# Kernel tuning notes

Hardware: AMD Instinct MI355X
Metric: run time of the kernel (lower is better)

## Reference

```python
import jax, jax.numpy as jnp
import numpy as np

# Mamba3/SSD selective state-space mixer (scalar-A-per-head SSD recurrence,
# causal depthwise conv on x/B/C, gated RMSNorm, in/out projections).
D_MODEL = 1024
EXPAND = 2
D_INNER = EXPAND * D_MODEL            # 2048
HEADDIM = D_MODEL // 16               # 64  (head_count=16 -> headdim 64)
NHEADS = D_INNER // HEADDIM           # 32
D_STATE = 128
CONV_W = 4
CONV_DIM = D_INNER + 2 * D_STATE      # x, B, C share the conv
D_IN_PROJ = 2 * D_INNER + 2 * D_STATE + NHEADS  # z, x, B, C, dt
EPS = 1e-5


def setup_inputs() -> dict:
    key = jax.random.key(0)
    ks = jax.random.split(key, 8)
    B, L = 4, 2048
    hidden = jax.random.normal(ks[0], (B, L, D_MODEL), dtype=jnp.float32)
    W_in = jax.random.normal(ks[1], (D_MODEL, D_IN_PROJ), dtype=jnp.float32) * 0.02
    conv_w = jax.random.normal(ks[2], (CONV_DIM, CONV_W), dtype=jnp.float32) * 0.2
    conv_b = jnp.zeros((CONV_DIM,), dtype=jnp.float32)
    # dt_bias: inverse-softplus of dt ~ U[1e-3, 0.1]
    dt = jnp.exp(jax.random.uniform(ks[3], (NHEADS,)) * (np.log(0.1) - np.log(1e-3)) + np.log(1e-3))
    dt_bias = dt + jnp.log(-jnp.expm1(-dt))
    A_log = jnp.log(jax.random.uniform(ks[4], (NHEADS,), minval=1.0, maxval=16.0))
    D = jnp.ones((NHEADS,), dtype=jnp.float32)
    norm_w = jnp.ones((D_INNER,), dtype=jnp.float32)
    W_out = jax.random.normal(ks[5], (D_INNER, D_MODEL), dtype=jnp.float32) * 0.02
    return {"hidden": hidden, "W_in": W_in, "conv_w": conv_w, "conv_b": conv_b,
            "dt_bias": dt_bias, "A_log": A_log, "D": D, "norm_w": norm_w, "W_out": W_out}


def _silu(x):
    return x * jax.nn.sigmoid(x)


def _mixer(hidden, W_in, conv_w, conv_b, dt_bias, A_log, D, norm_w, W_out):
    Bsz, L, _ = hidden.shape
    zxbcdt = hidden @ W_in                                    # [B,L,D_IN_PROJ]
    z = zxbcdt[..., :D_INNER]
    xBC = zxbcdt[..., D_INNER:D_INNER + CONV_DIM]
    dt = zxbcdt[..., -NHEADS:]                                # [B,L,H]
    # causal depthwise conv, width 4 (small fixed loop over taps)
    xp = jnp.pad(xBC, ((0, 0), (CONV_W - 1, 0), (0, 0)))
    conv = sum(xp[:, k:k + L, :] * conv_w[:, k] for k in range(CONV_W))
    xBC = _silu(conv + conv_b)
    x = xBC[..., :D_INNER].reshape(Bsz, L, NHEADS, HEADDIM)   # [B,L,H,P]
    Bm = xBC[..., D_INNER:D_INNER + D_STATE]                  # [B,L,N]
    Cm = xBC[..., D_INNER + D_STATE:]                         # [B,L,N]
    dt = jax.nn.softplus(dt + dt_bias)                        # [B,L,H]
    dA = jnp.exp(dt * (-jnp.exp(A_log)))                      # [B,L,H] decay in (0,1)
    dBx = jnp.einsum('blh,bln,blhp->blhpn', dt, Bm, x)        # [B,L,H,P,N]

    def step(h, inp):
        dA_t, dBx_t, C_t = inp                                # [B,H],[B,H,P,N],[B,N]
        h = dA_t[:, :, None, None] * h + dBx_t
        y = jnp.einsum('bhpn,bn->bhp', h, C_t)
        return h, y

    h0 = jnp.zeros((Bsz, NHEADS, HEADDIM, D_STATE), dtype=hidden.dtype)
    xs = (jnp.moveaxis(dA, 1, 0), jnp.moveaxis(dBx, 1, 0), jnp.moveaxis(Cm, 1, 0))
    _, ys = jax.lax.scan(step, h0, xs)                        # [L,B,H,P]
    y = jnp.moveaxis(ys, 0, 1) + D[None, None, :, None] * x   # skip term
    y = y.reshape(Bsz, L, D_INNER)
    # gated RMSNorm: norm(y * silu(z))
    y = y * _silu(z)
    y = y * jax.lax.rsqrt(jnp.mean(y * y, axis=-1, keepdims=True) + EPS) * norm_w
    return y @ W_out


def reference(hidden, W_in, conv_w, conv_b, dt_bias, A_log, D, norm_w, W_out):
    return _mixer(hidden, W_in, conv_w, conv_b, dt_bias, A_log, D, norm_w, W_out)
```

## Files before the change

kernel.cpp:

```cpp
#include <hip/hip_runtime.h>
#include <math.h>

#define BSZ 4
#define LEN 2048
#define DM 1024
#define DI 2048
#define HD 64
#define NH 32
#define DS 128
#define CD 2304
#define DP 4384
#define NTOK (BSZ*LEN)
#define QCH 128
#define NCH (LEN/QCH)
#define TOFF (DP-NH)

#define CONV_R 64
#define NRB (NTOK/CONV_R)
#define NPAD 4352

typedef unsigned short ushort_t;
typedef __bf16 bf16x8 __attribute__((ext_vector_type(8)));
typedef ushort_t us8 __attribute__((ext_vector_type(8)));
typedef float f32x4 __attribute__((ext_vector_type(4)));

__device__ __forceinline__ ushort_t f2bf(float f) {
    unsigned u = __float_as_uint(f);
    unsigned r = (u + 0x7FFFu + ((u >> 16) & 1u)) >> 16;
    return (ushort_t)r;
}
__device__ __forceinline__ float bf2f(ushort_t u) {
    return __uint_as_float(((unsigned)u) << 16);
}
__device__ __forceinline__ bf16x8 us2bf(us8 v) {
    union { us8 u; bf16x8 b; } x; x.u = v; return x.b;
}

__device__ __forceinline__ void gl_lds16(const void* g, void* l) {
    __builtin_amdgcn_global_load_lds(
        (const __attribute__((address_space(1))) void*)g,
        (__attribute__((address_space(3))) void*)l, 16, 0, 0);
}

__global__ __launch_bounds__(256) void cvt_bf16(
    const float* __restrict__ A, ushort_t* __restrict__ Ab)
{
    size_t i = ((size_t)blockIdx.x * 256 + threadIdx.x) * 4;
    float4 v = *(const float4*)(A + i);
    ushort_t o[4] = { f2bf(v.x), f2bf(v.y), f2bf(v.z), f2bf(v.w) };
    *(uint2*)(Ab + i) = *(uint2*)o;
}

__global__ __launch_bounds__(256) void transpose_cvt(
    const float* __restrict__ W, ushort_t* __restrict__ Wt,
    const float* __restrict__ colscale, int K, int N, int ldw)
{
    __shared__ float T[32][33];
    const int n0 = blockIdx.x * 32;
    const int k0 = blockIdx.y * 32;
    const int tid = threadIdx.x;
    #pragma unroll
    for (int l = 0; l < 4; l++) {
        int idx = tid + l * 256;
        int ki = idx >> 5, nj = idx & 31;
        int n = n0 + nj;
        float s = colscale ? colscale[k0 + ki] : 1.f;
        T[ki][nj] = (n < N) ? W[(size_t)(k0 + ki) * ldw + n] * s : 0.f;
    }
    __syncthreads();
    #pragma unroll
    for (int l = 0; l < 4; l++) {
        int idx = tid + l * 256;
        int nj = idx >> 5, ki = idx & 31;
        Wt[(size_t)(n0 + nj) * K + k0 + ki] = f2bf(T[ki][nj]);
    }
}

__global__ __launch_bounds__(512, 2) void gemm1_256(
    const ushort_t* __restrict__ A, const ushort_t* __restrict__ Bt,
    ushort_t* __restrict__ C, int K, int lda, int ldb, int ldc)
{
    __shared__ __align__(16) ushort_t LA[2][2][128 * 64];
    __shared__ __align__(16) ushort_t LB[2][2][128 * 64];
    const int tid = threadIdx.x;
    int bid = blockIdx.y * gridDim.x + blockIdx.x;
    const int nwg = gridDim.x * gridDim.y;
    if (!(nwg & 7)) bid = (bid & 7) * (nwg >> 3) + (bid >> 3);
    const int n0 = (bid % gridDim.x) * 256;
    const int m0 = (bid / gridDim.x) * 256;
    const int lane = tid & 63;
    const int w = tid >> 6;
    const int wm = w >> 2, wn = w & 3;
    const int lm = lane & 15, quad = lane >> 4;
    const int swz = (lm & 7) << 4;
    const int ck0 = ((0 * 64 + quad * 16) ^ swz) >> 1;
    const int ck1 = ((1 * 64 + quad * 16) ^ swz) >> 1;

    const int srow = tid >> 3;
    const int scolb = ((tid & 7) * 16) ^ (((tid >> 3) & 7) << 4);
    const char* gA = (const char*)A + ((size_t)(m0 + srow) * lda) * 2 + scolb;
    const char* gB = (const char*)Bt + ((size_t)(n0 + srow) * ldb) * 2 + scolb;
    const size_t strA = (size_t)64 * lda * 2;
    const size_t strB = (size_t)64 * ldb * 2;
    const int ldst = tid * 8;

    f32x4 acc[8][4];
    #pragma unroll
    for (int i = 0; i < 8; i++)
        #pragma unroll
        for (int j = 0; j < 4; j++) acc[i][j] = (f32x4){0.f, 0.f, 0.f, 0.f};

    const int NTt = K >> 6;

    {
        const char* a = gA;
        const char* b = gB;
        #pragma unroll
        for (int i = 0; i < 4; i++)
            gl_lds16(a + i * strA, &LA[0][i >> 1][(i & 1) * 4096 + ldst]);
        #pragma unroll
        for (int i = 0; i < 4; i++)
            gl_lds16(b + i * strB, &LB[0][i >> 1][(i & 1) * 4096 + ldst]);
    }
    __syncthreads();

    for (int kt = 0; kt < NTt; ++kt) {
        const int cur = kt & 1;
        if (kt + 1 < NTt) {
            const char* a = gA + (size_t)(kt + 1) * 128;
            const char* b = gB + (size_t)(kt + 1) * 128;
            const int nxt = cur ^ 1;
            #pragma unroll
            for (int i = 0; i < 4; i++)
                gl_lds16(a + i * strA, &LA[nxt][i >> 1][(i & 1) * 4096 + ldst]);
            #pragma unroll
            for (int i = 0; i < 4; i++)
                gl_lds16(b + i * strB, &LB[nxt][i >> 1][(i & 1) * 4096 + ldst]);
        }
        #pragma unroll
        for (int mq = 0; mq < 2; mq++) {
            bf16x8 af[4][2];
            #pragma unroll
            for (int m4 = 0; m4 < 4; m4++) {
                const int rbase = ((mq * 4 + m4) * 16 + lm) << 6;
                af[m4][0] = *(const bf16x8*)&LA[cur][wm][rbase + ck0];
                af[m4][1] = *(const bf16x8*)&LA[cur][wm][rbase + ck1];
            }
            #pragma unroll
            for (int nq = 0; nq < 2; nq++) {
                bf16x8 bfr[2][2];
                #pragma unroll
                for (int n2 = 0; n2 < 2; n2++) {
                    const int rbase = ((wn & 1) * 64 + (nq * 2 + n2) * 16 + lm) << 6;
                    bfr[n2][0] = *(const bf16x8*)&LB[cur][wn >> 1][rbase + ck0];
                    bfr[n2][1] = *(const bf16x8*)&LB[cur][wn >> 1][rbase + ck1];
                }
                __builtin_amdgcn_s_setprio(1);
                #pragma unroll
                for (int kk = 0; kk < 2; kk++)
                    #pragma unroll
                    for (int m4 = 0; m4 < 4; m4++)
                        #pragma unroll
                        for (int n2 = 0; n2 < 2; n2++)
                            acc[mq * 4 + m4][nq * 2 + n2] =
                                __builtin_amdgcn_mfma_f32_16x16x32_bf16(
                                    af[m4][kk], bfr[n2][kk],
                                    acc[mq * 4 + m4][nq * 2 + n2], 0, 0, 0);
                __builtin_amdgcn_s_setprio(0);
            }
        }
        if (kt + 1 < NTt) __syncthreads();
    }

    #pragma unroll
    for (int mf = 0; mf < 8; mf++) {
        const int row = m0 + wm * 128 + mf * 16 + quad * 4;
        #pragma unroll
        for (int nf = 0; nf < 4; nf++) {
            const int col = n0 + wn * 64 + nf * 16 + lm;
            #pragma unroll
            for (int r = 0; r < 4; r++)
                C[(size_t)(row + r) * ldc + col] = f2bf(acc[mf][nf][r]);
        }
    }
}

template <bool OB>
__global__ __launch_bounds__(256) void gemm_bf16(
    const ushort_t* __restrict__ A, const ushort_t* __restrict__ Bt,
    void* __restrict__ Cp, const float* __restrict__ rowscale,
    int K, int lda, int ldb, int ldc, int nmax)
{
    __shared__ __align__(16) ushort_t As[128 * 32];
    __shared__ __align__(16) ushort_t Bs[128 * 32];
    const int tid = threadIdx.x;
    int bid = blockIdx.y * gridDim.x + blockIdx.x;
    const int nwg = gridDim.x * gridDim.y;
    if (!(nwg & 7)) bid = (bid & 7) * (nwg >> 3) + (bid >> 3);
    const int n0 = (bid % gridDim.x) * 128;
    const int m0 = (bid / gridDim.x) * 128;
    const int lane = tid & 63;
    const int w = tid >> 6;
    const int wm = w >> 1, wn = w & 1;
    const int lm = lane & 15, quad = lane >> 4;

    const int srow = tid >> 2;
    const int skq = (tid & 3) * 8;
    const ushort_t* ga0 = A + (size_t)(m0 + srow) * lda + skq;
    const ushort_t* ga1 = A + (size_t)(m0 + 64 + srow) * lda + skq;
    const ushort_t* gb0 = Bt + (size_t)(n0 + srow) * ldb + skq;
    const ushort_t* gb1 = Bt + (size_t)(n0 + 64 + srow) * ldb + skq;
    ushort_t* la0 = &As[srow * 32 + skq];
    ushort_t* la1 = &As[(64 + srow) * 32 + skq];
    ushort_t* lb0 = &Bs[srow * 32 + skq];
    ushort_t* lb1 = &Bs[(64 + srow) * 32 + skq];

    f32x4 acc[4][4];
    #pragma unroll
    for (int i = 0; i < 4; i++)
        #pragma unroll
        for (int j = 0; j < 4; j++) acc[i][j] = (f32x4){0.f, 0.f, 0.f, 0.f};

    for (int k0 = 0; k0 < K; k0 += 32) {
        gl_lds16(ga0, la0);
        gl_lds16(ga1, la1);
        gl_lds16(gb0, lb0);
        gl_lds16(gb1, lb1);
        ga0 += 32; ga1 += 32; gb0 += 32; gb1 += 32;
        __syncthreads();
        bf16x8 af[4], bfr[4];
        #pragma unroll
        for (int i = 0; i < 4; i++)
            af[i] = *(const bf16x8*)&As[(wm * 64 + i * 16 + lm) * 32 + quad * 8];
        #pragma unroll
        for (int j = 0; j < 4; j++)
            bfr[j] = *(const bf16x8*)&Bs[(wn * 64 + j * 16 + lm) * 32 + quad * 8];
        #pragma unroll
        for (int i = 0; i < 4; i++)
            #pragma unroll
            for (int j = 0; j < 4; j++)
                acc[i][j] = __builtin_amdgcn_mfma_f32_16x16x32_bf16(af[i], bfr[j], acc[i][j], 0, 0, 0);
        __syncthreads();
    }

    #pragma unroll
    for (int i = 0; i < 4; i++) {
        int row = m0 + wm * 64 + i * 16 + quad * 4;
        float rs[4] = {1.f, 1.f, 1.f, 1.f};
        if (rowscale) {
            #pragma unroll
            for (int r = 0; r < 4; r++) rs[r] = rowscale[row + r];
        }
        #pragma unroll
        for (int j = 0; j < 4; j++) {
            int col = n0 + wn * 64 + j * 16 + lm;
            if (col < nmax) {
                #pragma unroll
                for (int r = 0; r < 4; r++) {
                    if (OB)
                        ((ushort_t*)Cp)[(size_t)(row + r) * ldc + col] = f2bf(acc[i][j][r] * rs[r]);
                    else
                        ((float*)Cp)[(size_t)(row + r) * ldc + col] = acc[i][j][r] * rs[r];
                }
            }
        }
    }
}

__global__ __launch_bounds__(256) void conv_silu_bf16(
    const ushort_t* __restrict__ xbcb, const float* __restrict__ cw,
    const float* __restrict__ cb, ushort_t* __restrict__ xT,
    ushort_t* __restrict__ Bn, ushort_t* __restrict__ BT,
    ushort_t* __restrict__ Cn)
{
    __shared__ ushort_t Tl[256][68];
    const int tid = threadIdx.x;
    const int c = blockIdx.x * 256 + tid;
    const int rb = blockIdx.y;
    const int row0 = rb * CONV_R;
    const bool isBC = (blockIdx.x == 8);

    const float w0 = cw[c*4+0], w1 = cw[c*4+1], w2 = cw[c*4+2], w3 = cw[c*4+3];
    const float bias = cb[c];
    float h0 = 0.f, h1 = 0.f, h2 = 0.f;
    if ((row0 & (LEN - 1)) != 0) {
        h0 = bf2f(xbcb[(size_t)(row0 - 3) * NPAD + c]);
        h1 = bf2f(xbcb[(size_t)(row0 - 2) * NPAD + c]);
        h2 = bf2f(xbcb[(size_t)(row0 - 1) * NPAD + c]);
    }
    const ushort_t* p = xbcb + (size_t)row0 * NPAD + c;
    for (int r = 0; r < CONV_R; r++) {
        float xin = bf2f(*p);
        float a = bias + w0*h0 + w1*h1 + w2*h2 + w3*xin;
        ushort_t bv = f2bf(a / (1.f + __expf(-a)));
        Tl[tid][r] = bv;
        if (isBC) {
            int row = row0 + r;
            if (tid < DS) Bn[(size_t)row * DS + tid] = bv;
            else          Cn[(size_t)row * DS + (tid - DS)] = bv;
        }
        h0 = h1; h1 = h2; h2 = xin;
        p += NPAD;
    }
    __syncthreads();

    const int seg = tid & 7;
    const int clb = tid >> 3;
    if (!isBC) {
        #pragma unroll
        for (int pass = 0; pass < 8; pass++) {
            int cl = pass * 32 + clb;
            int cc = blockIdx.x * 256 + cl;
            us8 v;
            #pragma unroll
            for (int j = 0; j < 8; j++) v[j] = Tl[cl][seg * 8 + j];
            *(us8*)&xT[(size_t)cc * NTOK + row0 + seg * 8] = v;
        }
    } else {
        #pragma unroll
        for (int pass = 0; pass < 4; pass++) {
            int n = pass * 32 + clb;
            us8 v;
            #pragma unroll
            for (int j = 0; j < 8; j++) v[j] = Tl[n][seg * 8 + j];
            *(us8*)&BT[(size_t)n * NTOK + row0 + seg * 8] = v;
        }
    }
}

__global__ __launch_bounds__(256) void gct_gemm(
    const ushort_t* __restrict__ Bn, const ushort_t* __restrict__ Cn,
    float* __restrict__ Graw)
{
    const int bc = blockIdx.x;
    const int chunk = bc % NCH;
    const int b = bc / NCH;
    const size_t rowbase = (size_t)b * LEN + (size_t)chunk * QCH;
    const int tid = threadIdx.x;
    const int w = tid >> 6, lane = tid & 63;
    const int lm = lane & 15, quad = lane >> 4;
    const int tw0 = w * 32;

    f32x4 acc[2][8];
    #pragma unroll
    for (int ti = 0; ti < 2; ti++)
        #pragma unroll
        for (int sj = 0; sj < 8; sj++) acc[ti][sj] = (f32x4){0.f, 0.f, 0.f, 0.f};

    #pragma unroll
    for (int ks = 0; ks < 4; ks++) {
        const int k0 = ks * 32 + quad * 8;
        bf16x8 a0 = *(const bf16x8*)&Cn[(rowbase + tw0 + lm) * DS + k0];
        bf16x8 a1 = *(const bf16x8*)&Cn[(rowbase + tw0 + 16 + lm) * DS + k0];
        #pragma unroll
        for (int sj = 0; sj < 8; sj++) {
            bf16x8 bb = *(const bf16x8*)&Bn[(rowbase + sj * 16 + lm) * DS + k0];
            acc[0][sj] = __builtin_amdgcn_mfma_f32_16x16x32_bf16(a0, bb, acc[0][sj], 0, 0, 0);
            acc[1][sj] = __builtin_amdgcn_mfma_f32_16x16x32_bf16(a1, bb, acc[1][sj], 0, 0, 0);
        }
    }
    float* G = Graw + (size_t)bc * (QCH * QCH);
    #pragma unroll
    for (int ti = 0; ti < 2; ti++)
        #pragma unroll
        for (int sj = 0; sj < 8; sj++)
            #pragma unroll
            for (int r = 0; r < 4; r++)
                G[(size_t)(tw0 + ti * 16 + quad * 4 + r) * QCH + sj * 16 + lm] = acc[ti][sj][r];
}

__global__ __launch_bounds__(256) void dt_proc_fp32(
    const float* __restrict__ hidden, const float* __restrict__ W_in,
    const float* __restrict__ dt_bias, const float* __restrict__ A_log,
    float* __restrict__ dtv, float* __restrict__ ldA)
{
    const int h = threadIdx.x & 31;
    const int tt = threadIdx.x >> 5;
    const int t = blockIdx.x * 8 + tt;
    const float* hr = hidden + (size_t)t * DM;
    const float* wc = W_in + TOFF + h;
    float a0 = 0.f, a1 = 0.f, a2 = 0.f, a3 = 0.f;
    for (int k = 0; k < DM; k += 4) {
        a0 += hr[k+0] * wc[(size_t)(k+0) * DP];
        a1 += hr[k+1] * wc[(size_t)(k+1) * DP];
        a2 += hr[k+2] * wc[(size_t)(k+2) * DP];
        a3 += hr[k+3] * wc[(size_t)(k+3) * DP];
    }
    float v = (a0 + a1) + (a2 + a3) + dt_bias[h];
    float sp = (v > 20.f) ? v : log1pf(expf(v));
    int idx = t * NH + h;
    dtv[idx] = sp;
    ldA[idx] = -sp * expf(A_log[h]);
}

__global__ __launch_bounds__(64) void scan_chunk(
    const float* __restrict__ dtv, const float* __restrict__ ldA,
    float* __restrict__ lcpb, float* __restrict__ dtsb,
    float* __restrict__ coefb, float* __restrict__ csum)
{
    const int blk = blockIdx.x;
    const int chunk = blk % NCH;
    const int bh = blk / NCH;
    const int h = bh % NH;
    const int b = bh / NH;
    const int lane = threadIdx.x;
    const size_t rowbase = (size_t)b * LEN + (size_t)chunk * QCH;
    const int t0 = 2 * lane, t1 = 2 * lane + 1;
    float v0 = ldA[(rowbase + t0) * NH + h];
    float v1 = ldA[(rowbase + t1) * NH + h];
    float d0 = dtv[(rowbase + t0) * NH + h];
    float d1 = dtv[(rowbase + t1) * NH + h];
    float pair = v0 + v1;
    #pragma unroll
    for (int off = 1; off < 64; off <<= 1) {
        float n = __shfl_up(pair, off, 64);
        if (lane >= off) pair += n;
    }
    float l1 = pair, l0 = pair - v1;
    float total = __shfl(pair, 63, 64);
    size_t base = (size_t)blk * QCH;
    *(float2*)&lcpb[base + t0] = make_float2(l0, l1);
    *(float2*)&dtsb[base + t0] = make_float2(d0, d1);
    *(float2*)&coefb[base + t0] =
        make_float2(__expf(total - l0) * d0, __expf(total - l1) * d1);
    if (lane == 63) csum[blk] = total;
}

__global__ __launch_bounds__(256) void phase1_mfma(
    const ushort_t* __restrict__ xT, const ushort_t* __restrict__ BT,
    const float* __restrict__ coefb, float* __restrict__ S)
{
    const int h = blockIdx.x & (NH - 1);
    const int bc = blockIdx.x >> 5;
    const int chunk = bc % NCH;
    const int b = bc / NCH;
    const int blko = (b * NH + h) * NCH + chunk;
    const int tid = threadIdx.x;
    const size_t rowbase = (size_t)b * LEN + (size_t)chunk * QCH;

    __shared__ float coef[QCH];
    if (tid < QCH) coef[tid] = coefb[(size_t)blko * QCH + tid];
    __syncthreads();

    const int w = tid >> 6, lane = tid & 63;
    const int lm = lane & 15, quad = lane >> 4;
    const int nw0 = w * 32;

    f32x4 acc[4][2];
    #pragma unroll
    for (int i = 0; i < 4; i++)
        #pragma unroll
        for (int j = 0; j < 2; j++) acc[i][j] = (f32x4){0.f, 0.f, 0.f, 0.f};

    #pragma unroll
    for (int ks = 0; ks < 4; ks++) {
        const int k0 = ks * 32 + quad * 8;
        bf16x8 a[4];
        #pragma unroll
        for (int mi = 0; mi < 4; mi++)
            a[mi] = *(const bf16x8*)&xT[(size_t)(h * HD + mi * 16 + lm) * NTOK + rowbase + k0];
        float cf[8];
        #pragma unroll
        for (int j = 0; j < 8; j++) cf[j] = coef[k0 + j];
        #pragma unroll
        for (int ni = 0; ni < 2; ni++) {
            us8 raw = *(const us8*)&BT[(size_t)(nw0 + ni * 16 + lm) * NTOK + rowbase + k0];
            us8 sb;
            #pragma unroll
            for (int j = 0; j < 8; j++) sb[j] = f2bf(bf2f(raw[j]) * cf[j]);
            bf16x8 bfr = us2bf(sb);
            __builtin_amdgcn_s_setprio(1);
            #pragma unroll
            for (int mi = 0; mi < 4; mi++)
                acc[mi][ni] = __builtin_amdgcn_mfma_f32_16x16x32_bf16(a[mi], bfr, acc[mi][ni], 0, 0, 0);
            __builtin_amdgcn_s_setprio(0);
        }
    }
    float* Sb = S + (size_t)blko * (HD * DS);
    #pragma unroll
    for (int mi = 0; mi < 4; mi++)
        #pragma unroll
        for (int ni = 0; ni < 2; ni++)
            #pragma unroll
            for (int r = 0; r < 4; r++)
                Sb[(size_t)(mi * 16 + quad * 4 + r) * DS + nw0 + ni * 16 + lm] = acc[mi][ni][r];
}

__global__ __launch_bounds__(256) void phase2(
    const float* __restrict__ S, const float* __restrict__ csum,
    ushort_t* __restrict__ hsb)
{
    const int bh = blockIdx.x >> 3;
    const int esl = blockIdx.x & 7;
    const int tid = threadIdx.x;
    const int eb = esl * 1024 + tid;
    float run[4] = {0.f, 0.f, 0.f, 0.f};
    for (int c = 0; c < NCH; c++) {
        float P = __expf(csum[bh * NCH + c]);
        size_t base = (size_t)(bh * NCH + c) * (HD * DS);
        #pragma unroll
        for (int i = 0; i < 4; i++) {
            size_t idx = base + eb + i * 256;
            float s = S[idx];
            hsb[idx] = f2bf(run[i]);
            run[i] = P * run[i] + s;
        }
    }
}

__global__ __launch_bounds__(256) void phase3_mfma(
    const ushort_t* __restrict__ xT, const ushort_t* __restrict__ Cn,
    const ushort_t* __restrict__ hsb, const float* __restrict__ Graw,
    const float* __restrict__ lcpb, const float* __restrict__ dtsb,
    const float* __restrict__ Dvec, ushort_t* __restrict__ zxb,
    float* __restrict__ ss)
{
    const int tid = threadIdx.x;
    const int h = blockIdx.x & (NH - 1);
    const int bc = blockIdx.x >> 5;
    const int chunk = bc % NCH;
    const int b = bc / NCH;
    const int blko = (b * NH + h) * NCH + chunk;
    const size_t rowbase = (size_t)b * LEN + (size_t)chunk * QCH;

    __shared__ float lcp[QCH];
    __shared__ float dts[QCH];
    if (tid < QCH) {
        lcp[tid] = lcpb[(size_t)blko * QCH + tid];
        dts[tid] = dtsb[(size_t)blko * QCH + tid];
    }
    __syncthreads();

    const int w = tid >> 6, lane = tid & 63;
    const int lm = lane & 15, quad = lane >> 4;
    const int tw0 = w * 32;

    const float* Gr = Graw + (size_t)bc * (QCH * QCH);
    const ushort_t* hsp = hsb + (size_t)blko * (HD * DS);

    f32x4 acc2[2][4];
    #pragma unroll
    for (int ti = 0; ti < 2; ti++)
        #pragma unroll
        for (int pi = 0; pi < 4; pi++) acc2[ti][pi] = (f32x4){0.f, 0.f, 0.f, 0.f};

    #pragma unroll
    for (int ks = 0; ks < 8; ks++) {
        bf16x8 a[2], bb[4];
        if (ks < 4) {
            const int k0 = ks * 32 + quad * 8;
            #pragma unroll
            for (int ti = 0; ti < 2; ti++) {
                int t = tw0 + ti * 16 + lm;
                float lt = lcp[t];
                const float* gp = Gr + (size_t)t * QCH + k0;
                float4 g0 = *(const float4*)gp;
                float4 g1 = *(const float4*)(gp + 4);
                float ge[8] = { g0.x, g0.y, g0.z, g0.w, g1.x, g1.y, g1.z, g1.w };
                us8 sb;
                #pragma unroll
                for (int j = 0; j < 8; j++) {
                    int s = k0 + j;
                    float wv = (s <= t) ? (__expf(lt - lcp[s]) * dts[s]) : 0.f;
                    sb[j] = f2bf(ge[j] * wv);
                }
                a[ti] = us2bf(sb);
            }
            #pragma unroll
            for (int pi = 0; pi < 4; pi++)
                bb[pi] = *(const bf16x8*)&xT[(size_t)(h * HD + pi * 16 + lm) * NTOK + rowbase + k0];
        } else {
            const int k0 = (ks - 4) * 32 + quad * 8;
            #pragma unroll
            for (int ti = 0; ti < 2; ti++) {
                int t = tw0 + ti * 16 + lm;
                float sc = __expf(lcp[t]);
                us8 raw = *(const us8*)&Cn[(rowbase + t) * DS + k0];
                us8 sb;
                #pragma unroll
                for (int j = 0; j < 8; j++) sb[j] = f2bf(bf2f(raw[j]) * sc);
                a[ti] = us2bf(sb);
            }
            #pragma unroll
            for (int pi = 0; pi < 4; pi++)
                bb[pi] = *(const bf16x8*)&hsp[(size_t)(pi * 16 + lm) * DS + k0];
        }
        __builtin_amdgcn_s_setprio(1);
        #pragma unroll
        for (int ti = 0; ti < 2; ti++)
            #pragma unroll
            for (int pi = 0; pi < 4; pi++)
                acc2[ti][pi] = __builtin_amdgcn_mfma_f32_16x16x32_bf16(a[ti], bb[pi], acc2[ti][pi], 0, 0, 0);
        __builtin_amdgcn_s_setprio(0);
    }

    const float Dh = Dvec[h];
    float vsq[2][4] = {};
    #pragma unroll
    for (int ti = 0; ti < 2; ti++)
        #pragma unroll
        for (int pi = 0; pi < 4; pi++) {
            int tb = tw0 + ti * 16 + quad * 4;
            int col = h * HD + pi * 16 + lm;
            ushort4 xv = *(const ushort4*)&xT[(size_t)(h * HD + pi * 16 + lm) * NTOK + rowbase + tb];
            const ushort_t* xe = (const ushort_t*)&xv;
            #pragma unroll
            for (int r = 0; r < 4; r++) {
                size_t grow = rowbase + tb + r;
                float y = acc2[ti][pi][r] + Dh * bf2f(xe[r]);
                float z = bf2f(zxb[grow * NPAD + col]);
                float v = y * (z / (1.f + __expf(-z)));
                vsq[ti][r] += v * v;
                zxb[grow * NPAD + DI + col] = f2bf(v);
            }
        }
    #pragma unroll
    for (int ti = 0; ti < 2; ti++)
        #pragma unroll
        for (int r = 0; r < 4; r++) {
            float s = vsq[ti][r];
            s += __shfl_xor(s, 1, 64);
            s += __shfl_xor(s, 2, 64);
            s += __shfl_xor(s, 4, 64);
            s += __shfl_xor(s, 8, 64);
            if (lm == 0) {
                int tb = tw0 + ti * 16 + quad * 4 + r;
                atomicAdd(&ss[rowbase + tb], s);
            }
        }
}

__global__ __launch_bounds__(256) void rms_finalize(
    const float* __restrict__ ss, float* __restrict__ rr)
{
    int t = blockIdx.x * 256 + threadIdx.x;
    rr[t] = rsqrtf(ss[t] * (1.f / DI) + 1e-5f);
}

extern "C" void kernel_launch(void* const* d_in, const int* in_sizes, int n_in,
                              void* d_out, int out_size, void* d_ws, size_t ws_size,
                              hipStream_t stream)
{
    const float* hidden  = (const float*)d_in[0];
    const float* W_in    = (const float*)d_in[1];
    const float* conv_w  = (const float*)d_in[2];
    const float* conv_b  = (const float*)d_in[3];
    const float* dt_bias = (const float*)d_in[4];
    const float* A_log   = (const float*)d_in[5];
    const float* Dv      = (const float*)d_in[6];
    const float* norm_w  = (const float*)d_in[7];
    const float* W_out   = (const float*)d_in[8];
    float* out = (float*)d_out;

    char* ws = (char*)d_ws;
    size_t o = 0;
    ushort_t* zxb  = (ushort_t*)(ws + o); o += (size_t)NTOK * NPAD * 2;
    float* S       = (float*)(ws + o);    o += (size_t)BSZ * NH * NCH * HD * DS * 4;
    ushort_t* xT   = (ushort_t*)(ws + o); o += (size_t)DI * NTOK * 2;
    ushort_t* Bn   = (ushort_t*)(ws + o); o += (size_t)NTOK * DS * 2;
    ushort_t* BT   = (ushort_t*)(ws + o); o += (size_t)DS * NTOK * 2;
    ushort_t* Cn   = (ushort_t*)(ws + o); o += (size_t)NTOK * DS * 2;
    ushort_t* hsb  = (ushort_t*)(ws + o); o += (size_t)BSZ * NH * NCH * HD * DS * 2;
    float* Graw    = (float*)(ws + o);    o += (size_t)BSZ * NCH * QCH * QCH * 4;
    float* dtv     = (float*)(ws + o);    o += (size_t)NTOK * NH * 4;
    float* ldA     = (float*)(ws + o);    o += (size_t)NTOK * NH * 4;
    float* lcpb    = (float*)(ws + o);    o += (size_t)BSZ * NH * LEN * 4;
    float* dtsb    = (float*)(ws + o);    o += (size_t)BSZ * NH * LEN * 4;
    float* coefb   = (float*)(ws + o);    o += (size_t)BSZ * NH * LEN * 4;
    float* csum    = (float*)(ws + o);    o += (size_t)BSZ * NH * NCH * 4;
    float* ss      = (float*)(ws + o);    o += (size_t)NTOK * 4;
    float* rr      = (float*)(ws + o);    o += (size_t)NTOK * 4;
    ushort_t* Ah   = (ushort_t*)S;
    ushort_t* W1t  = (ushort_t*)((char*)S + (size_t)NTOK * DM * 2);
    ushort_t* Wot  = hsb;
    ushort_t* xbcb = zxb + DI;
    ushort_t* ynb  = zxb + DI;

    hipMemsetAsync(ss, 0, (size_t)NTOK * 4, stream);
    cvt_bf16<<<(NTOK * DM) / 1024, 256, 0, stream>>>(hidden, Ah);
    transpose_cvt<<<dim3(NPAD / 32, DM / 32), 256, 0, stream>>>(
        W_in, W1t, nullptr, DM, NPAD, DP);
    gemm1_256<<<dim3(NPAD / 256, NTOK / 256), 512, 0, stream>>>(
        Ah, W1t, zxb, DM, DM, DM, NPAD);
    conv_silu_bf16<<<dim3(CD / 256, NRB), 256, 0, stream>>>(
        xbcb, conv_w, conv_b, xT, Bn, BT, Cn);
    gct_gemm<<<BSZ * NCH, 256, 0, stream>>>(Bn, Cn, Graw);
    dt_proc_fp32<<<NTOK / 8, 256, 0, stream>>>(hidden, W_in, dt_bias, A_log, dtv, ldA);
    scan_chunk<<<BSZ * NH * NCH, 64, 0, stream>>>(dtv, ldA, lcpb, dtsb, coefb, csum);
    phase1_mfma<<<BSZ * NH * NCH, 256, 0, stream>>>(xT, BT, coefb, S);
    phase2<<<BSZ * NH * 8, 256, 0, stream>>>(S, csum, hsb);
    phase3_mfma<<<BSZ * NH * NCH, 256, 0, stream>>>(
        xT, Cn, hsb, Graw, lcpb, dtsb, Dv, zxb, ss);
    rms_finalize<<<NTOK / 256, 256, 0, stream>>>(ss, rr);
    transpose_cvt<<<dim3(DM / 32, DI / 32), 256, 0, stream>>>(
        W_out, Wot, norm_w, DI, DM, DM);
    gemm_bf16<false><<<dim3(DM / 128, NTOK / 128), 256, 0, stream>>>(
        ynb, Wot, out, rr, DI, NPAD, DI, DM, DM);
}
```

Baseline: 532.5 us.

## Split GEMM main loop into half-tile phases with fine-grained vmcnt waits

Restructures the 256x256 in-projection GEMM inner loop so each warp computes across both LDS halves of A and B, with the tile mapping remapped to match. Global-to-LDS loads are reordered so the second A half is issued last, and the loop waits on partial vmcnt counts with raw barriers instead of full __syncthreads. The first half's MFMAs can then start while the second A half is still arriving. This relies on exact vmcnt counts matching the issue order, so any change to the load count would break correctness.

Measured after the change: 530.9 us. About the same (-0.3%).

```diff
diff --git a/kernel.cpp b/kernel.cpp
--- a/kernel.cpp
+++ b/kernel.cpp
@@ -112,72 +112,113 @@
 
     const int NTt = K >> 6;
 
-    {
-        const char* a = gA;
-        const char* b = gB;
-        #pragma unroll
-        for (int i = 0; i < 4; i++)
-            gl_lds16(a + i * strA, &LA[0][i >> 1][(i & 1) * 4096 + ldst]);
-        #pragma unroll
-        for (int i = 0; i < 4; i++)
-            gl_lds16(b + i * strB, &LB[0][i >> 1][(i & 1) * 4096 + ldst]);
-    }
-    __syncthreads();
+    auto STAGE = [&](int kt1, int nxt) {
+        const char* a = gA + (size_t)kt1 * 128;
+        const char* b = gB + (size_t)kt1 * 128;
+        gl_lds16(a + 0 * strA, &LA[nxt][0][0 * 4096 + ldst]);
+        gl_lds16(a + 1 * strA, &LA[nxt][0][1 * 4096 + ldst]);
+        gl_lds16(b + 0 * strB, &LB[nxt][0][0 * 4096 + ldst]);
+        gl_lds16(b + 1 * strB, &LB[nxt][0][1 * 4096 + ldst]);
+        gl_lds16(b + 2 * strB, &LB[nxt][1][0 * 4096 + ldst]);
+        gl_lds16(b + 3 * strB, &LB[nxt][1][1 * 4096 + ldst]);
+        asm volatile("" ::: "memory");
+        gl_lds16(a + 2 * strA, &LA[nxt][1][0 * 4096 + ldst]);
+        gl_lds16(a + 3 * strA, &LA[nxt][1][1 * 4096 + ldst]);
+    };
+
+    STAGE(0, 0);
 
     for (int kt = 0; kt < NTt; ++kt) {
         const int cur = kt & 1;
-        if (kt + 1 < NTt) {
-            const char* a = gA + (size_t)(kt + 1) * 128;
-            const char* b = gB + (size_t)(kt + 1) * 128;
-            const int nxt = cur ^ 1;
-            #pragma unroll
-            for (int i = 0; i < 4; i++)
-                gl_lds16(a + i * strA, &LA[nxt][i >> 1][(i & 1) * 4096 + ldst]);
-            #pragma unroll
-            for (int i = 0; i < 4; i++)
-                gl_lds16(b + i * strB, &LB[nxt][i >> 1][(i & 1) * 4096 + ldst]);
-        }
-        #pragma unroll
-        for (int mq = 0; mq < 2; mq++) {
-            bf16x8 af[4][2];
-            #pragma unroll
-            for (int m4 = 0; m4 < 4; m4++) {
-                const int rbase = ((mq * 4 + m4) * 16 + lm) << 6;
-                af[m4][0] = *(const bf16x8*)&LA[cur][wm][rbase + ck0];
-                af[m4][1] = *(const bf16x8*)&LA[cur][wm][rbase + ck1];
-            }
-            #pragma unroll
-            for (int nq = 0; nq < 2; nq++) {
-                bf16x8 bfr[2][2];
+        const bool last = (kt == NTt - 1);
+
+        asm volatile("s_waitcnt vmcnt(2)" ::: "memory");
+        __builtin_amdgcn_s_barrier();
+        if (!last) STAGE(kt + 1, cur ^ 1);
+
+        const ushort_t* Ah0 = &LA[cur][0][0];
+        const ushort_t* Ah1 = &LA[cur][1][0];
+        const ushort_t* Bh0 = &LB[cur][0][0];
+        const ushort_t* Bh1 = &LB[cur][1][0];
+
+        bf16x8 af[4][2], b0[2][2], b1[2][2];
+        #pragma unroll
+        for (int s = 0; s < 4; s++) {
+            const int rb = (wm * 64 + s * 16 + lm) << 6;
+            af[s][0] = *(const bf16x8*)&Ah0[rb + ck0];
+            af[s][1] = *(const bf16x8*)&Ah0[rb + ck1];
+        }
+        #pragma unroll
+        for (int t = 0; t < 2; t++) {
+            const int rb = (wn * 32 + t * 16 + lm) << 6;
+            b0[t][0] = *(const bf16x8*)&Bh0[rb + ck0];
+            b0[t][1] = *(const bf16x8*)&Bh0[rb + ck1];
+        }
+        __builtin_amdgcn_s_setprio(1);
+        #pragma unroll
+        for (int kk = 0; kk < 2; kk++)
+            #pragma unroll
+            for (int s = 0; s < 4; s++)
                 #pragma unroll
-                for (int n2 = 0; n2 < 2; n2++) {
-                    const int rbase = ((wn & 1) * 64 + (nq * 2 + n2) * 16 + lm) << 6;
-                    bfr[n2][0] = *(const bf16x8*)&LB[cur][wn >> 1][rbase + ck0];
-                    bfr[n2][1] = *(const bf16x8*)&LB[cur][wn >> 1][rbase + ck1];
-                }
-                __builtin_amdgcn_s_setprio(1);
+                for (int t = 0; t < 2; t++)
+                    acc[s][t] = __builtin_amdgcn_mfma_f32_16x16x32_bf16(
+                        af[s][kk], b0[t][kk], acc[s][t], 0, 0, 0);
+        __builtin_amdgcn_s_setprio(0);
+        #pragma unroll
+        for (int t = 0; t < 2; t++) {
+            const int rb = (wn * 32 + t * 16 + lm) << 6;
+            b1[t][0] = *(const bf16x8*)&Bh1[rb + ck0];
+            b1[t][1] = *(const bf16x8*)&Bh1[rb + ck1];
+        }
+        __builtin_amdgcn_s_setprio(1);
+        #pragma unroll
+        for (int kk = 0; kk < 2; kk++)
+            #pragma unroll
+            for (int s = 0; s < 4; s++)
                 #pragma unroll
-                for (int kk = 0; kk < 2; kk++)
-                    #pragma unroll
-                    for (int m4 = 0; m4 < 4; m4++)
-                        #pragma unroll
-                        for (int n2 = 0; n2 < 2; n2++)
-                            acc[mq * 4 + m4][nq * 2 + n2] =
-                                __builtin_amdgcn_mfma_f32_16x16x32_bf16(
-                                    af[m4][kk], bfr[n2][kk],
-                                    acc[mq * 4 + m4][nq * 2 + n2], 0, 0, 0);
-                __builtin_amdgcn_s_setprio(0);
-            }
-        }
-        if (kt + 1 < NTt) __syncthreads();
+                for (int t = 0; t < 2; t++)
+                    acc[s][2 + t] = __builtin_amdgcn_mfma_f32_16x16x32_bf16(
+                        af[s][kk], b1[t][kk], acc[s][2 + t], 0, 0, 0);
+        __builtin_amdgcn_s_setprio(0);
+
+        if (!last) asm volatile("s_waitcnt vmcnt(8)" ::: "memory");
+        else       asm volatile("s_waitcnt vmcnt(0)" ::: "memory");
+        __builtin_amdgcn_s_barrier();
+
+        #pragma unroll
+        for (int s = 0; s < 4; s++) {
+            const int rb = (wm * 64 + s * 16 + lm) << 6;
+            af[s][0] = *(const bf16x8*)&Ah1[rb + ck0];
+            af[s][1] = *(const bf16x8*)&Ah1[rb + ck1];
+        }
+        __builtin_amdgcn_s_setprio(1);
+        #pragma unroll
+        for (int kk = 0; kk < 2; kk++)
+            #pragma unroll
+            for (int s = 0; s < 4; s++)
+                #pragma unroll
+                for (int t = 0; t < 2; t++)
+                    acc[4 + s][t] = __builtin_amdgcn_mfma_f32_16x16x32_bf16(
+                        af[s][kk], b0[t][kk], acc[4 + s][t], 0, 0, 0);
+        __builtin_amdgcn_s_setprio(0);
+        __builtin_amdgcn_s_setprio(1);
+        #pragma unroll
+        for (int kk = 0; kk < 2; kk++)
+            #pragma unroll
+            for (int s = 0; s < 4; s++)
+                #pragma unroll
+                for (int t = 0; t < 2; t++)
+                    acc[4 + s][2 + t] = __builtin_amdgcn_mfma_f32_16x16x32_bf16(
+                        af[s][kk], b1[t][kk], acc[4 + s][2 + t], 0, 0, 0);
+        __builtin_amdgcn_s_setprio(0);
     }
 
     #pragma unroll
     for (int mf = 0; mf < 8; mf++) {
-        const int row = m0 + wm * 128 + mf * 16 + quad * 4;
+        const int row = m0 + (mf >> 2) * 128 + wm * 64 + (mf & 3) * 16 + quad * 4;
         #pragma unroll
         for (int nf = 0; nf < 4; nf++) {
-            const int col = n0 + wn * 64 + nf * 16 + lm;
+            const int col = n0 + (nf >> 1) * 128 + wn * 32 + (nf & 1) * 16 + lm;
             #pragma unroll
             for (int r = 0; r < 4; r++)
                 C[(size_t)(row + r) * ldc + col] = f2bf(acc[mf][nf][r]);
```
